# Kernel optimization log

Measured on AMD Instinct MI355X. Metric: run time of the kernel, lower is better.

Reference implementation:

```python
import jax, jax.numpy as jnp
import numpy as np

D_MODEL = 2048
HIDDEN = 1024
NUM_EXPERTS = 8
TOTAL_TOKENS = 16384  # tokens already sorted/grouped by expert


def setup_inputs() -> dict:
    key = jax.random.key(0)
    k1, k2, k3 = jax.random.split(key, 3)
    x = jax.random.normal(k1, (TOTAL_TOKENS, D_MODEL), dtype=jnp.float32)
    # nn.Linear(d_model, 2*E*H).weight -> [2*E*H, d_model]
    w_up_gate = jax.random.normal(k2, (2 * NUM_EXPERTS * HIDDEN, D_MODEL), dtype=jnp.float32) / np.sqrt(D_MODEL)
    # nn.Linear(E*H, d_model).weight -> [d_model, E*H]
    w_down = jax.random.normal(k3, (D_MODEL, NUM_EXPERTS * HIDDEN), dtype=jnp.float32) / np.sqrt(HIDDEN)
    batch_size_per_expert = jnp.full((NUM_EXPERTS,), TOTAL_TOKENS // NUM_EXPERTS, dtype=jnp.int32)
    return {
        "x": x,
        "w_up_gate": w_up_gate,
        "w_down": w_down,
        "batch_size_per_expert": batch_size_per_expert,
        "num_experts": NUM_EXPERTS,
    }


def reference(x, w_up_gate, w_down, batch_size_per_expert, num_experts):
    # Per-expert sizes are host constants (a Python list in the torch code).
    sizes = np.asarray(batch_size_per_expert)
    offs = np.concatenate([[0], np.cumsum(sizes)])  # static token offsets
    d_model = x.shape[-1]
    hidden = w_up_gate.shape[0] // (2 * num_experts)
    # [E, 2H, d_model]: expert e's fused up/gate weight block
    w_ug = w_up_gate.reshape(num_experts, 2 * hidden, d_model)
    outs = []
    for e in range(num_experts):  # small static loop over experts (ragged grouped GEMM)
        xe = x[offs[e]:offs[e + 1]]                      # [n_e, d_model]
        ug = xe @ w_ug[e].T                              # [n_e, 2H]
        h = jax.nn.silu(ug[:, :hidden]) * ug[:, hidden:]  # SwiGLU, [n_e, H]
        wd_e = w_down[:, e * hidden:(e + 1) * hidden]    # [d_model, H]
        outs.append(h @ wd_e.T)                          # [n_e, d_model]
    return jnp.concatenate(outs, axis=0)
```

## Files before the change

kernel.cpp:

```cpp
#include <hip/hip_runtime.h>
#include <hip/hip_bf16.h>

typedef __attribute__((ext_vector_type(8))) short short8;
typedef __attribute__((ext_vector_type(4))) float float4v;

#define BM 128
#define BK 32
#define LDSK 40

struct alignas(8) BF4 { unsigned short x, y, z, w; };
struct alignas(16) BF8 { unsigned short s[8]; };
struct alignas(16) I4 { int x, y, z, w; };

__device__ __forceinline__ unsigned short f2bf(float f) {
    union { float f; unsigned u; } v; v.f = f;
    unsigned u = v.u + (0x7FFFu + ((v.u >> 16) & 1u));
    return (unsigned short)(u >> 16);
}

__device__ __forceinline__ int find_expert(const int* __restrict__ bspe, int row0) {
    int e = 0, off = 0;
    #pragma unroll
    for (int i = 0; i < 8; ++i) {
        int s = bspe[i];
        if (row0 < off + s) { e = i; break; }
        off += s;
    }
    return e;
}

__device__ __forceinline__ void gload_lds16(const unsigned short* g, unsigned short* l) {
    __builtin_amdgcn_global_load_lds(
        (const __attribute__((address_space(1))) void*)g,
        (__attribute__((address_space(3))) void*)l, 16, 0, 0);
}

__global__ __launch_bounds__(256) void f32_to_bf16(const float* __restrict__ src,
                                                   unsigned short* __restrict__ dst,
                                                   long n) {
    const long stride = (long)gridDim.x * 256 * 8;
    for (long i = ((long)blockIdx.x * 256 + threadIdx.x) * 8; i < n; i += stride) {
        const float4 v0 = *(const float4*)(src + i);
        const float4 v1 = *(const float4*)(src + i + 4);
        BF8 o;
        o.s[0] = f2bf(v0.x); o.s[1] = f2bf(v0.y); o.s[2] = f2bf(v0.z); o.s[3] = f2bf(v0.w);
        o.s[4] = f2bf(v1.x); o.s[5] = f2bf(v1.y); o.s[6] = f2bf(v1.z); o.s[7] = f2bf(v1.w);
        *(BF8*)(dst + i) = o;
    }
}

#define BAR() __builtin_amdgcn_s_barrier()
#define WAITV(n) asm volatile("s_waitcnt vmcnt(" #n ")" ::: "memory")
#define WAITL0() do { asm volatile("s_waitcnt lgkmcnt(0)" ::: "memory"); \
                      __builtin_amdgcn_sched_barrier(0); } while (0)

#define STG_A(tt, kss) do { \
    gload_lds16(pA0 + (long)(tt) * 64 + (kss) * 32, As + ((((tt)&1)*2 + (kss))*8192) + 0*4096 + w*512); \
    gload_lds16(pA1 + (long)(tt) * 64 + (kss) * 32, As + ((((tt)&1)*2 + (kss))*8192) + 1*4096 + w*512); \
} while (0)
#define STG_B(tt, kss) do { \
    gload_lds16(pB0 + (long)(tt) * 64 + (kss) * 32, Bs + ((((tt)&1)*2 + (kss))*8192) + 0*4096 + w*512); \
    gload_lds16(pB1 + (long)(tt) * 64 + (kss) * 32, Bs + ((((tt)&1)*2 + (kss))*8192) + 1*4096 + w*512); \
} while (0)

#define RD_A(buf_, ks_, mh_) do { \
    const unsigned short* _p = As + (((buf_)*2 + (ks_))*8192) + gA + (arow + (mh_)*64)*32; \
    a[0] = *(const short8*)(_p);        a[1] = *(const short8*)(_p + 512); \
    a[2] = *(const short8*)(_p + 1024); a[3] = *(const short8*)(_p + 1536); \
} while (0)
#define RD_B(buf_, ks_) do { \
    const unsigned short* _p = Bs + (((buf_)*2 + (ks_))*8192) + gA + brow*32; \
    b[0] = *(const short8*)(_p);        b[1] = *(const short8*)(_p + 512); \
    b[2] = *(const short8*)(_p + 1024); b[3] = *(const short8*)(_p + 1536); \
} while (0)

#define MMA(mh_) do { \
    __builtin_amdgcn_s_setprio(1); \
    _Pragma("unroll") \
    for (int _j = 0; _j < 4; ++_j) \
        _Pragma("unroll") \
        for (int _n = 0; _n < 4; ++_n) \
            acc[(mh_)*4 + _j][_n] = __builtin_amdgcn_mfma_f32_16x16x32_bf16(a[_j], b[_n], acc[(mh_)*4 + _j][_n], 0, 0, 0); \
    __builtin_amdgcn_s_setprio(0); \
} while (0)

#define KLOOP(NKT) \
    STG_A(0, 0); STG_B(0, 0); \
    STG_A(0, 1); STG_B(0, 1); \
    STG_A(1, 0); STG_B(1, 0); \
    WAITV(8); \
    BAR(); \
    for (int t = 0; t < (NKT); ++t) { \
        const int buf = t & 1; \
        short8 a[4], b[4]; \
         \
        RD_B(buf, 0); RD_A(buf, 0, 0); \
        if (t < (NKT) - 1) STG_A(t + 1, 1); \
        BAR(); WAITL0(); \
        MMA(0); \
        BAR(); \
         \
        RD_A(buf, 0, 1); \
        if (t < (NKT) - 1) { STG_B(t + 1, 1); WAITV(8); } else { WAITV(0); } \
        BAR(); WAITL0(); \
        MMA(1); \
        BAR(); \
         \
        RD_B(buf, 1); RD_A(buf, 1, 0); \
        if (t < (NKT) - 2) STG_A(t + 2, 0); \
        BAR(); WAITL0(); \
        MMA(0); \
        BAR(); \
         \
        RD_A(buf, 1, 1); \
        if (t < (NKT) - 2) { STG_B(t + 2, 0); WAITV(8); } \
        else if (t == (NKT) - 2) { WAITV(4); } \
        BAR(); WAITL0(); \
        MMA(1); \
        BAR(); \
    }

__global__ __launch_bounds__(512) void moe_up_gate_p8(
    const unsigned short* __restrict__ xb, const unsigned short* __restrict__ wb,
    const int* __restrict__ bspe, unsigned short* __restrict__ hws) {
    __shared__ alignas(16) unsigned short As[32768];
    __shared__ alignas(16) unsigned short Bs[32768];

    const int t0 = threadIdx.x;
    const int lane = t0 & 63;
    const int w = t0 >> 6;
    const int wr = w >> 2, wc = w & 3;
    const int row0 = blockIdx.y * 256;
    const int h0 = blockIdx.x * 128;
    const int e = find_expert(bspe, row0);

    const int srow = lane >> 2;
    const int gs = ((lane & 3) ^ ((lane >> 3) & 3)) * 8;
    const unsigned short* pA0 = xb + (long)(row0 + w * 16 + srow) * 2048 + gs;
    const unsigned short* pA1 = pA0 + (long)128 * 2048;
    const unsigned short* pB0; const unsigned short* pB1;
    {
        const int r0 = w * 16 + srow;
        const int r1 = r0 + 128;
        const int in0 = r0 & 63, in1 = r1 & 63;
        const long g0 = (long)e * 2048 + (in0 < 32 ? 0 : 1024) + h0 + (r0 >> 6) * 32 + (in0 & 31);
        const long g1 = (long)e * 2048 + (in1 < 32 ? 0 : 1024) + h0 + (r1 >> 6) * 32 + (in1 & 31);
        pB0 = wb + g0 * 2048 + gs;
        pB1 = wb + g1 * 2048 + gs;
    }

    const int l15 = lane & 15;
    const int gA = ((lane >> 4) ^ ((l15 >> 1) & 3)) * 8;
    const int arow = wr * 128 + l15;
    const int brow = wc * 64 + l15;

    float4v acc[8][4];
    #pragma unroll
    for (int m = 0; m < 8; ++m)
        #pragma unroll
        for (int n = 0; n < 4; ++n)
            acc[m][n] = (float4v){0.f, 0.f, 0.f, 0.f};

    KLOOP(32)

    const int rbase = row0 + wr * 128 + (lane >> 4) * 4;
    const int cbase = h0 + wc * 32 + l15;
    #pragma unroll
    for (int m = 0; m < 8; ++m)
        #pragma unroll
        for (int n = 0; n < 2; ++n)
            #pragma unroll
            for (int q = 0; q < 4; ++q) {
                const float u = acc[m][n][q];
                const float g = acc[m][n + 2][q];
                const float s = u / (1.f + __expf(-u));
                hws[(long)(rbase + m * 16 + q) * 1024 + cbase + n * 16] = f2bf(s * g);
            }
}

__global__ __launch_bounds__(512) void moe_down_p8(
    const unsigned short* __restrict__ hws, const unsigned short* __restrict__ wdb,
    const int* __restrict__ bspe, float* __restrict__ out) {
    __shared__ alignas(16) unsigned short As[32768];
    __shared__ alignas(16) unsigned short Bs[32768];

    const int t0 = threadIdx.x;
    const int lane = t0 & 63;
    const int w = t0 >> 6;
    const int wr = w >> 2, wc = w & 3;
    const int row0 = blockIdx.y * 256;
    const int n0 = blockIdx.x * 256;
    const int e = find_expert(bspe, row0);

    const int srow = lane >> 2;
    const int gs = ((lane & 3) ^ ((lane >> 3) & 3)) * 8;
    const unsigned short* pA0 = hws + (long)(row0 + w * 16 + srow) * 1024 + gs;
    const unsigned short* pA1 = pA0 + (long)128 * 1024;
    const unsigned short* pB0 = wdb + (long)(n0 + w * 16 + srow) * 8192 + (long)e * 1024 + gs;
    const unsigned short* pB1 = pB0 + (long)128 * 8192;

    const int l15 = lane & 15;
    const int gA = ((lane >> 4) ^ ((l15 >> 1) & 3)) * 8;
    const int arow = wr * 128 + l15;
    const int brow = wc * 64 + l15;

    float4v acc[8][4];
    #pragma unroll
    for (int m = 0; m < 8; ++m)
        #pragma unroll
        for (int n = 0; n < 4; ++n)
            acc[m][n] = (float4v){0.f, 0.f, 0.f, 0.f};

    KLOOP(16)

    const int rbase = row0 + wr * 128 + (lane >> 4) * 4;
    const int cbase = n0 + wc * 64 + l15;
    #pragma unroll
    for (int m = 0; m < 8; ++m)
        #pragma unroll
        for (int n = 0; n < 4; ++n)
            #pragma unroll
            for (int q = 0; q < 4; ++q)
                out[(long)(rbase + m * 16 + q) * 2048 + cbase + n * 16] = acc[m][n][q];
}

__device__ __forceinline__ void stage_f32_tile(const float* __restrict__ src, long ld,
                                               unsigned short* lds, int t) {
    const int rr  = t >> 3;
    const int col = (t & 7) << 2;
    #pragma unroll
    for (int r = 0; r < 4; ++r) {
        const int row = rr + r * 32;
        const float4 v = *(const float4*)(src + (long)row * ld + col);
        BF4 o; o.x = f2bf(v.x); o.y = f2bf(v.y); o.z = f2bf(v.z); o.w = f2bf(v.w);
        *(BF4*)(lds + row * LDSK + col) = o;
    }
}

__global__ __launch_bounds__(256) void moe_up_gate(
    const float* __restrict__ x, const float* __restrict__ wug,
    const int* __restrict__ bspe, unsigned short* __restrict__ hws) {
    __shared__ alignas(16) unsigned short As[BM * LDSK];
    __shared__ alignas(16) unsigned short Bs[BM * LDSK];

    const int t = threadIdx.x;
    const int lane = t & 63;
    const int w = t >> 6;
    const int wr = w >> 1, wc = w & 1;
    const int bm = blockIdx.y;
    const int h0 = blockIdx.x * 64;
    const int row0 = bm * BM;

    const int e = find_expert(bspe, row0);

    const float* abase = x + (long)row0 * 2048;
    const float* bup = wug + ((long)e * 2048 + h0) * 2048;
    const float* bgt = wug + ((long)e * 2048 + 1024 + h0) * 2048;

    float4v acc[4][4];
    #pragma unroll
    for (int m = 0; m < 4; ++m)
        #pragma unroll
        for (int n = 0; n < 4; ++n)
            acc[m][n] = (float4v){0.f, 0.f, 0.f, 0.f};

    const int k8 = (lane >> 4) << 3;
    const int am = wr * 64 + (lane & 15);
    const int l15 = lane & 15;

    for (int k0 = 0; k0 < 2048; k0 += BK) {
        __syncthreads();
        stage_f32_tile(abase + k0, 2048, As, t);
        {
            const int rr  = t >> 3;
            const int col = (t & 7) << 2;
            #pragma unroll
            for (int r = 0; r < 4; ++r) {
                const int row = rr + r * 32;
                const float* p = (row < 64 ? bup + (long)row * 2048
                                           : bgt + (long)(row - 64) * 2048) + k0 + col;
                const float4 v = *(const float4*)p;
                BF4 o; o.x = f2bf(v.x); o.y = f2bf(v.y); o.z = f2bf(v.z); o.w = f2bf(v.w);
                *(BF4*)(Bs + row * LDSK + col) = o;
            }
        }
        __syncthreads();

        short8 a[4], b[4];
        #pragma unroll
        for (int m = 0; m < 4; ++m)
            a[m] = *(const short8*)(As + (am + m * 16) * LDSK + k8);
        #pragma unroll
        for (int n = 0; n < 4; ++n) {
            const int rb = (n < 2) ? (wc * 32 + n * 16) : (64 + wc * 32 + (n - 2) * 16);
            b[n] = *(const short8*)(Bs + (rb + l15) * LDSK + k8);
        }
        #pragma unroll
        for (int m = 0; m < 4; ++m)
            #pragma unroll
            for (int n = 0; n < 4; ++n)
                acc[m][n] = __builtin_amdgcn_mfma_f32_16x16x32_bf16(a[m], b[n], acc[m][n], 0, 0, 0);
    }

    const int rbase = row0 + wr * 64 + (lane >> 4) * 4;
    const int cbase = h0 + wc * 32 + l15;
    #pragma unroll
    for (int m = 0; m < 4; ++m)
        #pragma unroll
        for (int n = 0; n < 2; ++n)
            #pragma unroll
            for (int q = 0; q < 4; ++q) {
                const float u = acc[m][n][q];
                const float g = acc[m][n + 2][q];
                const float s = u / (1.f + __expf(-u));
                hws[(long)(rbase + m * 16 + q) * 1024 + cbase + n * 16] = f2bf(s * g);
            }
}

__global__ __launch_bounds__(256) void moe_down(
    const unsigned short* __restrict__ hws, const float* __restrict__ wd,
    const int* __restrict__ bspe, float* __restrict__ out) {
    __shared__ alignas(16) unsigned short As[BM * LDSK];
    __shared__ alignas(16) unsigned short Bs[BM * LDSK];

    const int t = threadIdx.x;
    const int lane = t & 63;
    const int w = t >> 6;
    const int wr = w >> 1, wc = w & 1;
    const int bm = blockIdx.y;
    const int n0 = blockIdx.x * BM;
    const int row0 = bm * BM;

    const int e = find_expert(bspe, row0);

    const unsigned short* abase = hws + (long)row0 * 1024;
    const float* bbase = wd + (long)n0 * 8192 + e * 1024;

    float4v acc[4][4];
    #pragma unroll
    for (int m = 0; m < 4; ++m)
        #pragma unroll
        for (int n = 0; n < 4; ++n)
            acc[m][n] = (float4v){0.f, 0.f, 0.f, 0.f};

    const int k8 = (lane >> 4) << 3;
    const int am = wr * 64 + (lane & 15);
    const int l15 = lane & 15;

    for (int k0 = 0; k0 < 1024; k0 += BK) {
        __syncthreads();
        {
            const int row = t >> 2;
            const int col = (t & 3) << 3;
            #pragma unroll
            for (int r = 0; r < 2; ++r) {
                const I4 v = *(const I4*)(abase + (long)(row + r * 64) * 1024 + k0 + col);
                *(I4*)(As + (row + r * 64) * LDSK + col) = v;
            }
        }
        stage_f32_tile(bbase + k0, 8192, Bs, t);
        __syncthreads();

        short8 a[4], b[4];
        #pragma unroll
        for (int m = 0; m < 4; ++m)
            a[m] = *(const short8*)(As + (am + m * 16) * LDSK + k8);
        #pragma unroll
        for (int n = 0; n < 4; ++n)
            b[n] = *(const short8*)(Bs + (wc * 64 + n * 16 + l15) * LDSK + k8);
        #pragma unroll
        for (int m = 0; m < 4; ++m)
            #pragma unroll
            for (int n = 0; n < 4; ++n)
                acc[m][n] = __builtin_amdgcn_mfma_f32_16x16x32_bf16(a[m], b[n], acc[m][n], 0, 0, 0);
    }

    const int rbase = row0 + wr * 64 + (lane >> 4) * 4;
    const int cbase = n0 + wc * 64 + l15;
    #pragma unroll
    for (int m = 0; m < 4; ++m)
        #pragma unroll
        for (int n = 0; n < 4; ++n)
            #pragma unroll
            for (int q = 0; q < 4; ++q)
                out[(long)(rbase + m * 16 + q) * 2048 + cbase + n * 16] = acc[m][n][q];
}

extern "C" void kernel_launch(void* const* d_in, const int* in_sizes, int n_in,
                              void* d_out, int out_size, void* d_ws, size_t ws_size,
                              hipStream_t stream) {
    const float* x   = (const float*)d_in[0];
    const float* wug = (const float*)d_in[1];
    const float* wd  = (const float*)d_in[2];
    const int*  bspe = (const int*)d_in[3];
    float* out = (float*)d_out;

    const size_t SZ_XB  = 16384UL * 2048UL * 2UL;
    const size_t SZ_WB  = 16384UL * 2048UL * 2UL;
    const size_t SZ_H   = 16384UL * 1024UL * 2UL;
    const size_t NEED   = SZ_XB + SZ_WB + SZ_H;

    if (ws_size >= NEED) {
        unsigned short* xb  = (unsigned short*)d_ws;
        unsigned short* wb  = (unsigned short*)((char*)d_ws + SZ_XB);
        unsigned short* hws = (unsigned short*)((char*)d_ws + SZ_XB + SZ_WB);
        unsigned short* wdb = (unsigned short*)d_ws;

        f32_to_bf16<<<2048, 256, 0, stream>>>(x,   xb,  16384L * 2048L);
        f32_to_bf16<<<2048, 256, 0, stream>>>(wug, wb,  16384L * 2048L);
        moe_up_gate_p8<<<dim3(8, 64), dim3(512), 0, stream>>>(xb, wb, bspe, hws);
        f32_to_bf16<<<1024, 256, 0, stream>>>(wd,  wdb, 2048L * 8192L);
        moe_down_p8<<<dim3(8, 64), dim3(512), 0, stream>>>(hws, wdb, bspe, out);
    } else {
        unsigned short* hws = (unsigned short*)d_ws;
        moe_up_gate<<<dim3(16, 128), dim3(256), 0, stream>>>(x, wug, bspe, hws);
        moe_down  <<<dim3(16, 128), dim3(256), 0, stream>>>(hws, wd, bspe, out);
    }
}
```

Measured before the change: 589.6 us.

## Prefetch LDS fragments into double registers and fuse bf16 conversion launches

```diff
diff --git a/kernel.cpp b/kernel.cpp
--- a/kernel.cpp
+++ b/kernel.cpp
@@ -35,11 +35,11 @@
         (__attribute__((address_space(3))) void*)l, 16, 0, 0);
 }
 
-__global__ __launch_bounds__(256) void f32_to_bf16(const float* __restrict__ src,
-                                                   unsigned short* __restrict__ dst,
-                                                   long n) {
-    const long stride = (long)gridDim.x * 256 * 8;
-    for (long i = ((long)blockIdx.x * 256 + threadIdx.x) * 8; i < n; i += stride) {
+__device__ __forceinline__ void conv_body(const float* __restrict__ src,
+                                          unsigned short* __restrict__ dst,
+                                          long n, int b0, int nb) {
+    const long stride = (long)nb * 256 * 8;
+    for (long i = ((long)b0 * 256 + threadIdx.x) * 8; i < n; i += stride) {
         const float4 v0 = *(const float4*)(src + i);
         const float4 v1 = *(const float4*)(src + i + 4);
         BF8 o;
@@ -49,10 +49,33 @@
     }
 }
 
+__global__ __launch_bounds__(256) void f32_to_bf16(const float* __restrict__ src,
+                                                   unsigned short* __restrict__ dst,
+                                                   long n) {
+    conv_body(src, dst, n, blockIdx.x, gridDim.x);
+}
+
+__global__ __launch_bounds__(256) void convert2(const float* __restrict__ x, unsigned short* __restrict__ xb,
+                                                const float* __restrict__ wug, unsigned short* __restrict__ wb) {
+    const int b = blockIdx.x;
+    if (b < 2048) conv_body(x, xb, 16384L * 2048L, b, 2048);
+    else          conv_body(wug, wb, 16384L * 2048L, b - 2048, 2048);
+}
+
+__global__ __launch_bounds__(256) void convert3(const float* __restrict__ x, unsigned short* __restrict__ xb,
+                                                const float* __restrict__ wug, unsigned short* __restrict__ wb,
+                                                const float* __restrict__ wd, unsigned short* __restrict__ wdb) {
+    const int b = blockIdx.x;
+    if (b < 2048)      conv_body(x, xb, 16384L * 2048L, b, 2048);
+    else if (b < 4096) conv_body(wug, wb, 16384L * 2048L, b - 2048, 2048);
+    else               conv_body(wd, wdb, 2048L * 8192L, b - 4096, 1024);
+}
+
 #define BAR() __builtin_amdgcn_s_barrier()
-#define WAITV(n) asm volatile("s_waitcnt vmcnt(" #n ")" ::: "memory")
-#define WAITL0() do { asm volatile("s_waitcnt lgkmcnt(0)" ::: "memory"); \
+#define WAITV(n) do { asm volatile("s_waitcnt vmcnt(" #n ")" ::: "memory"); \
                       __builtin_amdgcn_sched_barrier(0); } while (0)
+#define WAITLC(n) do { asm volatile("s_waitcnt lgkmcnt(" #n ")" ::: "memory"); \
+                       __builtin_amdgcn_sched_barrier(0); } while (0)
 
 #define STG_A(tt, kss) do { \
     gload_lds16(pA0 + (long)(tt) * 64 + (kss) * 32, As + ((((tt)&1)*2 + (kss))*8192) + 0*4096 + w*512); \
@@ -63,60 +86,65 @@
     gload_lds16(pB1 + (long)(tt) * 64 + (kss) * 32, Bs + ((((tt)&1)*2 + (kss))*8192) + 1*4096 + w*512); \
 } while (0)
 
-#define RD_A(buf_, ks_, mh_) do { \
+#define RD_A4(dst, buf_, ks_, mh_) do { \
     const unsigned short* _p = As + (((buf_)*2 + (ks_))*8192) + gA + (arow + (mh_)*64)*32; \
-    a[0] = *(const short8*)(_p);        a[1] = *(const short8*)(_p + 512); \
-    a[2] = *(const short8*)(_p + 1024); a[3] = *(const short8*)(_p + 1536); \
+    dst[0] = *(const short8*)(_p);        dst[1] = *(const short8*)(_p + 512); \
+    dst[2] = *(const short8*)(_p + 1024); dst[3] = *(const short8*)(_p + 1536); \
 } while (0)
-#define RD_B(buf_, ks_) do { \
+#define RD_B4(dst, buf_, ks_) do { \
     const unsigned short* _p = Bs + (((buf_)*2 + (ks_))*8192) + gA + brow*32; \
-    b[0] = *(const short8*)(_p);        b[1] = *(const short8*)(_p + 512); \
-    b[2] = *(const short8*)(_p + 1024); b[3] = *(const short8*)(_p + 1536); \
+    dst[0] = *(const short8*)(_p);        dst[1] = *(const short8*)(_p + 512); \
+    dst[2] = *(const short8*)(_p + 1024); dst[3] = *(const short8*)(_p + 1536); \
 } while (0)
 
-#define MMA(mh_) do { \
+#define MMA_AB(A_, B_, mh_) do { \
     __builtin_amdgcn_s_setprio(1); \
     _Pragma("unroll") \
     for (int _j = 0; _j < 4; ++_j) \
         _Pragma("unroll") \
         for (int _n = 0; _n < 4; ++_n) \
-            acc[(mh_)*4 + _j][_n] = __builtin_amdgcn_mfma_f32_16x16x32_bf16(a[_j], b[_n], acc[(mh_)*4 + _j][_n], 0, 0, 0); \
+            acc[(mh_)*4 + _j][_n] = __builtin_amdgcn_mfma_f32_16x16x32_bf16(A_[_j], B_[_n], acc[(mh_)*4 + _j][_n], 0, 0, 0); \
     __builtin_amdgcn_s_setprio(0); \
 } while (0)
 
 #define KLOOP(NKT) \
+    short8 a0[4], a1[4], b0[4], b1[4]; \
     STG_A(0, 0); STG_B(0, 0); \
     STG_A(0, 1); STG_B(0, 1); \
     STG_A(1, 0); STG_B(1, 0); \
     WAITV(8); \
     BAR(); \
+    RD_B4(b0, 0, 0); RD_A4(a0, 0, 0, 0); \
     for (int t = 0; t < (NKT); ++t) { \
         const int buf = t & 1; \
-        short8 a[4], b[4]; \
          \
-        RD_B(buf, 0); RD_A(buf, 0, 0); \
         if (t < (NKT) - 1) STG_A(t + 1, 1); \
-        BAR(); WAITL0(); \
-        MMA(0); \
+        BAR(); \
+        RD_A4(a1, buf, 0, 1); \
+        WAITLC(4); \
+        MMA_AB(a0, b0, 0); \
         BAR(); \
          \
-        RD_A(buf, 0, 1); \
         if (t < (NKT) - 1) { STG_B(t + 1, 1); WAITV(8); } else { WAITV(0); } \
-        BAR(); WAITL0(); \
-        MMA(1); \
+        BAR(); \
+        RD_B4(b1, buf, 1); RD_A4(a0, buf, 1, 0); \
+        WAITLC(8); \
+        MMA_AB(a1, b0, 1); \
         BAR(); \
          \
-        RD_B(buf, 1); RD_A(buf, 1, 0); \
         if (t < (NKT) - 2) STG_A(t + 2, 0); \
-        BAR(); WAITL0(); \
-        MMA(0); \
+        BAR(); \
+        RD_A4(a1, buf, 1, 1); \
+        WAITLC(4); \
+        MMA_AB(a0, b1, 0); \
         BAR(); \
          \
-        RD_A(buf, 1, 1); \
         if (t < (NKT) - 2) { STG_B(t + 2, 0); WAITV(8); } \
         else if (t == (NKT) - 2) { WAITV(4); } \
-        BAR(); WAITL0(); \
-        MMA(1); \
+        BAR(); \
+        if (t < (NKT) - 1) { RD_B4(b0, buf ^ 1, 0); RD_A4(a0, buf ^ 1, 0, 0); WAITLC(8); } \
+        else { WAITLC(0); } \
+        MMA_AB(a1, b1, 1); \
         BAR(); \
     }
 
@@ -398,18 +426,28 @@
     const size_t SZ_XB  = 16384UL * 2048UL * 2UL;
     const size_t SZ_WB  = 16384UL * 2048UL * 2UL;
     const size_t SZ_H   = 16384UL * 1024UL * 2UL;
+    const size_t SZ_WD  = 2048UL * 8192UL * 2UL;
     const size_t NEED   = SZ_XB + SZ_WB + SZ_H;
-
-    if (ws_size >= NEED) {
+    const size_t NEED2  = SZ_XB + SZ_WB + SZ_H + SZ_WD;
+
+    if (ws_size >= NEED2) {
+        unsigned short* xb  = (unsigned short*)d_ws;
+        unsigned short* wb  = (unsigned short*)((char*)d_ws + SZ_XB);
+        unsigned short* hws = (unsigned short*)((char*)d_ws + SZ_XB + SZ_WB);
+        unsigned short* wdb = (unsigned short*)((char*)d_ws + SZ_XB + SZ_WB + SZ_H);
+
+        convert3<<<5120, 256, 0, stream>>>(x, xb, wug, wb, wd, wdb);
+        moe_up_gate_p8<<<dim3(8, 64), dim3(512), 0, stream>>>(xb, wb, bspe, hws);
+        moe_down_p8<<<dim3(8, 64), dim3(512), 0, stream>>>(hws, wdb, bspe, out);
+    } else if (ws_size >= NEED) {
         unsigned short* xb  = (unsigned short*)d_ws;
         unsigned short* wb  = (unsigned short*)((char*)d_ws + SZ_XB);
         unsigned short* hws = (unsigned short*)((char*)d_ws + SZ_XB + SZ_WB);
         unsigned short* wdb = (unsigned short*)d_ws;
 
-        f32_to_bf16<<<2048, 256, 0, stream>>>(x,   xb,  16384L * 2048L);
-        f32_to_bf16<<<2048, 256, 0, stream>>>(wug, wb,  16384L * 2048L);
+        convert2<<<4096, 256, 0, stream>>>(x, xb, wug, wb);
         moe_up_gate_p8<<<dim3(8, 64), dim3(512), 0, stream>>>(xb, wb, bspe, hws);
-        f32_to_bf16<<<1024, 256, 0, stream>>>(wd,  wdb, 2048L * 8192L);
+        f32_to_bf16<<<1024, 256, 0, stream>>>(wd, wdb, 2048L * 8192L);
         moe_down_p8<<<dim3(8, 64), dim3(512), 0, stream>>>(hws, wdb, bspe, out);
     } else {
         unsigned short* hws = (unsigned short*)d_ws;
```

Result: slower. 636.2 us (+7.9%).
